# Performance work log

Hardware: AMD Instinct MI355X
Metric: run time of the kernel (lower is better)

The kernel has to match this reference:

```python
import jax, jax.numpy as jnp
import numpy as np

MARGIN = 0.5
EPS = 1e-5


def setup_inputs() -> dict:
    key = jax.random.key(0)
    k1, k2 = jax.random.split(key)
    n, d, n_new, n_old = 8192, 256, 4096, 4096
    feature = jax.random.normal(k1, (n, d), dtype=jnp.float32)
    target = jax.random.randint(k2, (n,), 0, 100, dtype=jnp.int64)
    new_idx = jnp.arange(n_new, dtype=jnp.int64)
    old_idx = jnp.arange(n_old, dtype=jnp.int64)
    return {"feature": feature, "target": target, "new_idx": new_idx, "old_idx": old_idx}


def _triplet_loss(feature, target, new_idx, old_idx):
    n = feature.shape[0]
    n_new = new_idx.shape[0]
    # alpha switch is based on static shape, exactly as in the torch code
    alpha = 0.9 if old_idx.shape[0] != 0 else 0.5

    sim = feature @ feature.T                      # [n, n]
    sim_new = sim[:, new_idx]                      # [n, n_new]
    t_new = target[new_idx]                        # [n_new]

    same_new = target[:, None] == t_new[None, :]   # [n, n_new]
    is_new_row = jnp.arange(n) < n_new             # [n]

    # positive pairs (only defined for rows i < n_new)
    pos_mask = same_new & (sim_new < 1.0 - EPS)
    pos_loss_new = jnp.sum(jnp.where(pos_mask, 1.0 - sim_new, 0.0), axis=1)  # [n]
    # faithful to the torch bug: rows i >= n_new reuse the stale pos_pair_
    # from the last new row (i = n_new - 1)
    stale_pos = pos_loss_new[n_new - 1]
    pos_loss = jnp.where(is_new_row, pos_loss_new, stale_pos)

    # negatives: new rows scan all columns, old rows scan only new_idx columns
    diff_all = target[:, None] != target[None, :]
    neg_all = jnp.sum(jnp.where(diff_all & (sim > MARGIN), sim, 0.0), axis=1)
    neg_newcols = jnp.sum(jnp.where((~same_new) & (sim_new > MARGIN), sim_new, 0.0), axis=1)
    neg_loss = jnp.where(is_new_row, neg_all, neg_newcols)

    return jnp.mean(alpha * pos_loss + (1.0 - alpha) * neg_loss)


def reference(feature, target, new_idx, old_idx):
    return _triplet_loss(feature, target, new_idx, old_idx)
```

## Files before the change

### kernel.cpp

```cpp
#include <hip/hip_runtime.h>
#include <hip/hip_bf16.h>
#include <stdint.h>

#define MARGIN   0.5f
#define POS_THR  (1.0f - 1e-5f)

typedef __attribute__((ext_vector_type(8))) short  short8;
typedef __attribute__((ext_vector_type(4))) float  f32x4;

#define BM 128
#define BN 128
#define NSLOTS 256
#define MAXN_HIST 8192

__device__ __forceinline__ ushort f2bf_rne(float x) {
  uint32_t u = __float_as_uint(x);
  u += 0x7fffu + ((u >> 16) & 1u);
  return (ushort)(u >> 16);
}

__global__ __launch_bounds__(256) void prep_kernel(
    const float* __restrict__ src, ushort* __restrict__ dst,
    const int* __restrict__ target, const int* __restrict__ new_idx,
    int2* __restrict__ metaG, int* __restrict__ flags, float* __restrict__ misc,
    int total8, int n, int npanel, int n_new, int convBlocks) {
  const int tid = threadIdx.x;
  if ((int)blockIdx.x < convBlocks) {
    int i = blockIdx.x * blockDim.x + tid;
    if (i < total8) {
      const float4* s4 = reinterpret_cast<const float4*>(src);
      float4 a = s4[i * 2], b = s4[i * 2 + 1];
      short8 o;
      o[0] = (short)f2bf_rne(a.x); o[1] = (short)f2bf_rne(a.y);
      o[2] = (short)f2bf_rne(a.z); o[3] = (short)f2bf_rne(a.w);
      o[4] = (short)f2bf_rne(b.x); o[5] = (short)f2bf_rne(b.y);
      o[6] = (short)f2bf_rne(b.z); o[7] = (short)f2bf_rne(b.w);
      reinterpret_cast<short8*>(dst)[i] = o;
    }
    return;
  }
  __shared__ int hcnt[MAXN_HIST];
  __shared__ int hflag[MAXN_HIST / BN];
  for (int i = tid; i < n; i += 256) hcnt[i] = 0;
  for (int i = tid; i < npanel; i += 256) hflag[i] = 0;
  __syncthreads();
  for (int i = tid; i < n_new; i += 256) atomicAdd(&hcnt[new_idx[i]], 1);
  __syncthreads();
  for (int i = tid; i < n; i += 256) {
    int c = hcnt[i];
    metaG[i] = make_int2(target[i], __float_as_int((float)c));
    if (c) atomicOr(&hflag[i >> 7], 1);
  }
  __syncthreads();
  for (int i = tid; i < npanel; i += 256) flags[i] = hflag[i];
  for (int i = tid; i < NSLOTS + 1; i += 256) misc[i] = 0.f;
}

__global__ __launch_bounds__(256) void simloss_kernel(
    const ushort* __restrict__ fb, const int2* __restrict__ metaG,
    const int* __restrict__ flags, float* __restrict__ misc,
    int d, int n_new, float alpha) {
  __shared__ int2 metaR[BM];
  __shared__ int2 metaC[BN];
  __shared__ float red[4];

  const int l = blockIdx.x;
  int by = (int)((sqrtf(8.f * (float)l + 1.f) - 1.f) * 0.5f);
  while ((by + 1) * (by + 2) / 2 <= l) by++;
  while (by * (by + 1) / 2 > l) by--;
  const int bx = l - by * (by + 1) / 2;

  const int rowBase = by * BM;
  const int colBase = bx * BN;
  if ((rowBase >= n_new && flags[bx] == 0) &&
      (colBase >= n_new && flags[by] == 0)) return;

  const int tid  = threadIdx.x;
  const int lane = tid & 63;
  const int wid  = tid >> 6;
  const int wr   = wid >> 1;
  const int wc   = wid & 1;
  const int l15  = lane & 15;
  const int kb   = lane >> 4;

  if (tid < BM)        metaR[tid]       = metaG[rowBase + tid];
  else if (tid < 256)  metaC[tid - 128] = metaG[colBase + (tid - 128)];
  __syncthreads();

  const ushort* pA = fb + (size_t)(rowBase + wr * 64 + l15) * d + kb * 8;
  const ushort* pB = fb + (size_t)(colBase + wc * 64 + l15) * d + kb * 8;

  f32x4 acc[4][4] = {};
  const int nk = d >> 5;
#pragma unroll 2
  for (int ks = 0; ks < nk; ++ks) {
    short8 afr[4], bfr[4];
#pragma unroll
    for (int m = 0; m < 4; ++m)
      afr[m] = *reinterpret_cast<const short8*>(pA + (size_t)m * 16 * d + ks * 32);
#pragma unroll
    for (int nf = 0; nf < 4; ++nf)
      bfr[nf] = *reinterpret_cast<const short8*>(pB + (size_t)nf * 16 * d + ks * 32);
#pragma unroll
    for (int m = 0; m < 4; ++m)
#pragma unroll
      for (int nf = 0; nf < 4; ++nf)
        acc[m][nf] = __builtin_amdgcn_mfma_f32_16x16x32_bf16(bfr[nf], afr[m], acc[m][nf], 0, 0, 0);
  }

  const float beta = 1.0f - alpha;
  const bool diag = (bx == by);
  int tcr[4][4]; float cwc[4][4]; bool cnr[4][4];
#pragma unroll
  for (int nf = 0; nf < 4; ++nf)
#pragma unroll
    for (int q = 0; q < 4; ++q) {
      int cl = wc * 64 + nf * 16 + kb * 4 + q;
      int2 mc = metaC[cl];
      tcr[nf][q] = mc.x;
      cwc[nf][q] = __int_as_float(mc.y);
      cnr[nf][q] = (colBase + cl) < n_new;
    }

  const int  stale_row = n_new - 1;
  const bool blk_stale = (stale_row >= rowBase) && (stale_row < rowBase + BM);
  const int  srl = stale_row - rowBase;

  float tot = 0.f;
#pragma unroll
  for (int m = 0; m < 4; ++m) {
    int rl = wr * 64 + m * 16 + l15;
    int r  = rowBase + rl;
    int2 mr = metaR[rl];
    int   tr  = mr.x;
    float cwr = __int_as_float(mr.y);
    bool rnew = (r < n_new);
    float acwr = alpha * cwr, bcwr = beta * cwr;
    float p = 0.f, ng = 0.f, t2 = 0.f;
#pragma unroll
    for (int nf = 0; nf < 4; ++nf)
#pragma unroll
      for (int q = 0; q < 4; ++q) {
        float s = acc[m][nf][q];
        bool same = (tr == tcr[nf][q]);
        bool gm = (s > MARGIN);
        bool lp = (s < POS_THR);
        if (rnew) {
          if (same && lp)  p  += cwc[nf][q] * (1.0f - s);
          if (!same && gm) ng += s;
        } else {
          if (!same && gm) ng += cwc[nf][q] * s;
        }
        if (cnr[nf][q]) {
          if (same && lp)  t2 += acwr * (1.0f - s);
          if (!same && gm) t2 += beta * s;
        } else {
          if (!same && gm) t2 += bcwr * s;
        }
      }
    if (blk_stale && wr == (srl >> 6) && m == ((srl >> 4) & 3)) {
      float pr = p;
      pr += __shfl_xor(pr, 16); pr += __shfl_xor(pr, 32);
      if (lane < 16 && rl == srl) atomicAdd(&misc[NSLOTS], pr);
    }
    tot += rnew ? fmaf(alpha, p, beta * ng) : beta * ng;
    if (!diag) tot += t2;
  }
#pragma unroll
  for (int off = 32; off; off >>= 1) tot += __shfl_xor(tot, off);
  if (lane == 0) red[wid] = tot;
  __syncthreads();
  if (tid == 0)
    atomicAdd(&misc[blockIdx.x & (NSLOTS - 1)], red[0] + red[1] + red[2] + red[3]);
}

__global__ void finalize_kernel(const float* __restrict__ misc,
                                float* __restrict__ out, int n, int n_new,
                                float alpha) {
  int t = threadIdx.x;
  float c = misc[t] + misc[t + 64] + misc[t + 128] + misc[t + 192];
#pragma unroll
  for (int off = 32; off; off >>= 1) c += __shfl_xor(c, off);
  if (t == 0)
    out[0] = (c + (float)(n - n_new) * alpha * misc[NSLOTS]) / (float)n;
}

extern "C" void kernel_launch(void* const* d_in, const int* in_sizes, int n_in,
                              void* d_out, int out_size, void* d_ws, size_t ws_size,
                              hipStream_t stream) {
  const float* feature = (const float*)d_in[0];
  const int*   target  = (const int*)d_in[1];
  const int*   new_idx = (const int*)d_in[2];

  const int n     = in_sizes[1];
  const int d     = in_sizes[0] / n;
  const int n_new = in_sizes[2];
  const int n_old = (n_in > 3) ? in_sizes[3] : 0;
  const float alpha = (n_old != 0) ? 0.9f : 0.5f;
  const int npanel = n / BN;
  const int nTiles = npanel * (npanel + 1) / 2;

  auto al = [](size_t x) { return (x + 255) & ~(size_t)255; };
  char* ws = (char*)d_ws;
  ushort* fb    = (ushort*)ws;
  size_t  off   = al((size_t)n * d * sizeof(ushort));
  int2*   metaG = (int2*)(ws + off);  off += al((size_t)n * sizeof(int2));
  int*    flags = (int*)(ws + off);   off += al((size_t)npanel * sizeof(int));
  float*  misc  = (float*)(ws + off);

  int total8 = (n * d) / 8;
  int convBlocks = (total8 + 255) / 256;
  prep_kernel<<<convBlocks + 1, 256, 0, stream>>>(feature, fb, target, new_idx,
                                                  metaG, flags, misc,
                                                  total8, n, npanel, n_new,
                                                  convBlocks);

  simloss_kernel<<<nTiles, 256, 0, stream>>>(fb, metaG, flags, misc,
                                             d, n_new, alpha);

  finalize_kernel<<<1, 64, 0, stream>>>(misc, (float*)d_out, n, n_new, alpha);
}
```

Measured before the change: 150.1 us.

## Shrink tiles to 64x64 and stage full-K operands in swizzled LDS via async loads

Reduces the triangular tile size from 128 to 64. Each block now loads its whole 64x256 A and B panels into LDS with global_load_lds, using an XOR swizzle to avoid bank conflicts, and reuses the A panel on diagonal tiles. This replaces per-lane global fragment loads with shared-memory reads and creates four times as many blocks for occupancy. The costs are 64KB of LDS per block, which limits resident blocks, more blocks to launch, and less reuse per tile. The bf16 conversion also switches to nontemporal loads and stores.

```diff
diff --git a/kernel.cpp b/kernel.cpp
--- a/kernel.cpp
+++ b/kernel.cpp
@@ -8,8 +8,8 @@
 typedef __attribute__((ext_vector_type(8))) short  short8;
 typedef __attribute__((ext_vector_type(4))) float  f32x4;
 
-#define BM 128
-#define BN 128
+#define TM 64
+#define NPSHIFT 6
 #define NSLOTS 256
 #define MAXN_HIST 8192
 
@@ -17,6 +17,13 @@
   uint32_t u = __float_as_uint(x);
   u += 0x7fffu + ((u >> 16) & 1u);
   return (ushort)(u >> 16);
+}
+
+__device__ __forceinline__ void async_load16(const ushort* g, ushort* l) {
+  __builtin_amdgcn_global_load_lds(
+      (__attribute__((address_space(1))) void*)(const_cast<ushort*>(g)),
+      (__attribute__((address_space(3))) void*)(l),
+      16, 0, 0);
 }
 
 __global__ __launch_bounds__(256) void prep_kernel(
@@ -28,19 +35,20 @@
   if ((int)blockIdx.x < convBlocks) {
     int i = blockIdx.x * blockDim.x + tid;
     if (i < total8) {
-      const float4* s4 = reinterpret_cast<const float4*>(src);
-      float4 a = s4[i * 2], b = s4[i * 2 + 1];
+      const f32x4* s4 = reinterpret_cast<const f32x4*>(src);
+      f32x4 a = __builtin_nontemporal_load(&s4[i * 2]);
+      f32x4 b = __builtin_nontemporal_load(&s4[i * 2 + 1]);
       short8 o;
-      o[0] = (short)f2bf_rne(a.x); o[1] = (short)f2bf_rne(a.y);
-      o[2] = (short)f2bf_rne(a.z); o[3] = (short)f2bf_rne(a.w);
-      o[4] = (short)f2bf_rne(b.x); o[5] = (short)f2bf_rne(b.y);
-      o[6] = (short)f2bf_rne(b.z); o[7] = (short)f2bf_rne(b.w);
-      reinterpret_cast<short8*>(dst)[i] = o;
+      o[0] = (short)f2bf_rne(a[0]); o[1] = (short)f2bf_rne(a[1]);
+      o[2] = (short)f2bf_rne(a[2]); o[3] = (short)f2bf_rne(a[3]);
+      o[4] = (short)f2bf_rne(b[0]); o[5] = (short)f2bf_rne(b[1]);
+      o[6] = (short)f2bf_rne(b[2]); o[7] = (short)f2bf_rne(b[3]);
+      __builtin_nontemporal_store(o, &reinterpret_cast<short8*>(dst)[i]);
     }
     return;
   }
   __shared__ int hcnt[MAXN_HIST];
-  __shared__ int hflag[MAXN_HIST / BN];
+  __shared__ int hflag[MAXN_HIST / TM];
   for (int i = tid; i < n; i += 256) hcnt[i] = 0;
   for (int i = tid; i < npanel; i += 256) hflag[i] = 0;
   __syncthreads();
@@ -49,7 +57,7 @@
   for (int i = tid; i < n; i += 256) {
     int c = hcnt[i];
     metaG[i] = make_int2(target[i], __float_as_int((float)c));
-    if (c) atomicOr(&hflag[i >> 7], 1);
+    if (c) atomicOr(&hflag[i >> NPSHIFT], 1);
   }
   __syncthreads();
   for (int i = tid; i < npanel; i += 256) flags[i] = hflag[i];
@@ -60,8 +68,9 @@
     const ushort* __restrict__ fb, const int2* __restrict__ metaG,
     const int* __restrict__ flags, float* __restrict__ misc,
     int d, int n_new, float alpha) {
-  __shared__ int2 metaR[BM];
-  __shared__ int2 metaC[BN];
+  __shared__ __align__(16) ushort Als[TM * 256];
+  __shared__ __align__(16) ushort Bls[TM * 256];
+  __shared__ int2  metaR[TM], metaC[TM];
   __shared__ float red[4];
 
   const int l = blockIdx.x;
@@ -70,8 +79,9 @@
   while (by * (by + 1) / 2 > l) by--;
   const int bx = l - by * (by + 1) / 2;
 
-  const int rowBase = by * BM;
-  const int colBase = bx * BN;
+  const int rowBase = by * TM;
+  const int colBase = bx * TM;
+  const bool diag = (bx == by);
   if ((rowBase >= n_new && flags[bx] == 0) &&
       (colBase >= n_new && flags[by] == 0)) return;
 
@@ -83,53 +93,72 @@
   const int l15  = lane & 15;
   const int kb   = lane >> 4;
 
-  if (tid < BM)        metaR[tid]       = metaG[rowBase + tid];
-  else if (tid < 256)  metaC[tid - 128] = metaG[colBase + (tid - 128)];
-  __syncthreads();
-
-  const ushort* pA = fb + (size_t)(rowBase + wr * 64 + l15) * d + kb * 8;
-  const ushort* pB = fb + (size_t)(colBase + wc * 64 + l15) * d + kb * 8;
-
-  f32x4 acc[4][4] = {};
-  const int nk = d >> 5;
-#pragma unroll 2
-  for (int ks = 0; ks < nk; ++ks) {
-    short8 afr[4], bfr[4];
-#pragma unroll
-    for (int m = 0; m < 4; ++m)
-      afr[m] = *reinterpret_cast<const short8*>(pA + (size_t)m * 16 * d + ks * 32);
-#pragma unroll
-    for (int nf = 0; nf < 4; ++nf)
-      bfr[nf] = *reinterpret_cast<const short8*>(pB + (size_t)nf * 16 * d + ks * 32);
-#pragma unroll
-    for (int m = 0; m < 4; ++m)
-#pragma unroll
-      for (int nf = 0; nf < 4; ++nf)
+  if (tid < TM)           metaR[tid]      = metaG[rowBase + tid];
+  else if (tid < 2 * TM)  metaC[tid - TM] = metaG[colBase + (tid - TM)];
+
+#pragma unroll
+  for (int j = 0; j < 8; ++j) {
+    int L = j * 256 + tid;
+    int row = L >> 5, k = L & 31;
+    int cp = k ^ (row & 7);
+    async_load16(fb + (size_t)(rowBase + row) * d + cp * 8, &Als[(size_t)L * 8]);
+  }
+  if (!diag) {
+#pragma unroll
+    for (int j = 0; j < 8; ++j) {
+      int L = j * 256 + tid;
+      int row = L >> 5, k = L & 31;
+      int cp = k ^ (row & 7);
+      async_load16(fb + (size_t)(colBase + row) * d + cp * 8, &Bls[(size_t)L * 8]);
+    }
+  }
+  __syncthreads();
+  const ushort* Bbase = diag ? Als : Bls;
+
+  f32x4 acc[2][2] = {};
+#pragma unroll
+  for (int ks = 0; ks < 8; ++ks) {
+    short8 afr[2], bfr[2];
+#pragma unroll
+    for (int m = 0; m < 2; ++m) {
+      int row = wr * 32 + m * 16 + l15;
+      int c   = ks * 4 + kb;
+      afr[m] = *reinterpret_cast<const short8*>(&Als[row * 256 + ((c ^ (row & 7)) << 3)]);
+    }
+#pragma unroll
+    for (int nf = 0; nf < 2; ++nf) {
+      int row = wc * 32 + nf * 16 + l15;
+      int c   = ks * 4 + kb;
+      bfr[nf] = *reinterpret_cast<const short8*>(&Bbase[row * 256 + ((c ^ (row & 7)) << 3)]);
+    }
+#pragma unroll
+    for (int m = 0; m < 2; ++m)
+#pragma unroll
+      for (int nf = 0; nf < 2; ++nf)
         acc[m][nf] = __builtin_amdgcn_mfma_f32_16x16x32_bf16(bfr[nf], afr[m], acc[m][nf], 0, 0, 0);
   }
 
   const float beta = 1.0f - alpha;
-  const bool diag = (bx == by);
-  int tcr[4][4]; float cwc[4][4]; bool cnr[4][4];
-#pragma unroll
-  for (int nf = 0; nf < 4; ++nf)
+  int tcr[2][4]; float cwc_[2][4]; bool cnr[2][4];
+#pragma unroll
+  for (int nf = 0; nf < 2; ++nf)
 #pragma unroll
     for (int q = 0; q < 4; ++q) {
-      int cl = wc * 64 + nf * 16 + kb * 4 + q;
+      int cl = wc * 32 + nf * 16 + kb * 4 + q;
       int2 mc = metaC[cl];
-      tcr[nf][q] = mc.x;
-      cwc[nf][q] = __int_as_float(mc.y);
-      cnr[nf][q] = (colBase + cl) < n_new;
+      tcr[nf][q]  = mc.x;
+      cwc_[nf][q] = __int_as_float(mc.y);
+      cnr[nf][q]  = (colBase + cl) < n_new;
     }
 
   const int  stale_row = n_new - 1;
-  const bool blk_stale = (stale_row >= rowBase) && (stale_row < rowBase + BM);
+  const bool blk_stale = (stale_row >= rowBase) && (stale_row < rowBase + TM);
   const int  srl = stale_row - rowBase;
 
   float tot = 0.f;
 #pragma unroll
-  for (int m = 0; m < 4; ++m) {
-    int rl = wr * 64 + m * 16 + l15;
+  for (int m = 0; m < 2; ++m) {
+    int rl = wr * 32 + m * 16 + l15;
     int r  = rowBase + rl;
     int2 mr = metaR[rl];
     int   tr  = mr.x;
@@ -138,7 +167,7 @@
     float acwr = alpha * cwr, bcwr = beta * cwr;
     float p = 0.f, ng = 0.f, t2 = 0.f;
 #pragma unroll
-    for (int nf = 0; nf < 4; ++nf)
+    for (int nf = 0; nf < 2; ++nf)
 #pragma unroll
       for (int q = 0; q < 4; ++q) {
         float s = acc[m][nf][q];
@@ -146,10 +175,10 @@
         bool gm = (s > MARGIN);
         bool lp = (s < POS_THR);
         if (rnew) {
-          if (same && lp)  p  += cwc[nf][q] * (1.0f - s);
+          if (same && lp)  p  += cwc_[nf][q] * (1.0f - s);
           if (!same && gm) ng += s;
         } else {
-          if (!same && gm) ng += cwc[nf][q] * s;
+          if (!same && gm) ng += cwc_[nf][q] * s;
         }
         if (cnr[nf][q]) {
           if (same && lp)  t2 += acwr * (1.0f - s);
@@ -158,7 +187,7 @@
           if (!same && gm) t2 += bcwr * s;
         }
       }
-    if (blk_stale && wr == (srl >> 6) && m == ((srl >> 4) & 3)) {
+    if (blk_stale && wr == (srl >> 5) && m == ((srl >> 4) & 1)) {
       float pr = p;
       pr += __shfl_xor(pr, 16); pr += __shfl_xor(pr, 32);
       if (lane < 16 && rl == srl) atomicAdd(&misc[NSLOTS], pr);
@@ -171,7 +200,8 @@
   if (lane == 0) red[wid] = tot;
   __syncthreads();
   if (tid == 0)
-    atomicAdd(&misc[blockIdx.x & (NSLOTS - 1)], red[0] + red[1] + red[2] + red[3]);
+    atomicAdd(&misc[blockIdx.x & (NSLOTS - 1)],
+              red[0] + red[1] + red[2] + red[3]);
 }
 
 __global__ void finalize_kernel(const float* __restrict__ misc,
@@ -197,7 +227,7 @@
   const int n_new = in_sizes[2];
   const int n_old = (n_in > 3) ? in_sizes[3] : 0;
   const float alpha = (n_old != 0) ? 0.9f : 0.5f;
-  const int npanel = n / BN;
+  const int npanel = n / TM;
   const int nTiles = npanel * (npanel + 1) / 2;
 
   auto al = [](size_t x) { return (x + 255) & ~(size_t)255; };
```

Result: faster. 136.2 us (-9.2%).
